# Optimization experiments

Hardware: AMD Instinct MI355X
Metric: run time of the kernel (lower is better)

## Reference

```python
import jax, jax.numpy as jnp
import numpy as np

NUM_GRAPHS = 512


def setup_inputs() -> dict:
    key = jax.random.key(0)
    ks = jax.random.split(key, 16)
    N, E = 50000, 800000
    x = jax.random.normal(ks[0], (N, 3), dtype=jnp.float32)
    edge_index = jax.random.randint(ks[1], (2, E), 0, N, dtype=jnp.int64)
    batch = jnp.sort(jax.random.randint(ks[2], (N,), 0, NUM_GRAPHS, dtype=jnp.int64))

    def glorot(k, shape):
        fan_in, fan_out = shape
        lim = (6.0 / (fan_in + fan_out)) ** 0.5
        return jax.random.uniform(k, shape, jnp.float32, -lim, lim)

    return {
        "x": x, "edge_index": edge_index, "batch": batch,
        "W1": glorot(ks[3], (3, 32)),   "b1": jnp.zeros((32,), jnp.float32),
        "W2": glorot(ks[4], (32, 64)),  "b2": jnp.zeros((64,), jnp.float32),
        "W3": glorot(ks[5], (64, 128)), "b3": jnp.zeros((128,), jnp.float32),
        "Wf1": glorot(ks[6], (128, 32)), "bf1": jnp.zeros((32,), jnp.float32),
        "Wf2": glorot(ks[7], (32, 4)),   "bf2": jnp.zeros((4,), jnp.float32),
    }


def _gcn_conv(x, src, dst, norm, W, b, N):
    # GCNConv: h = x W, then symmetric-normalized aggregation, then bias.
    h = x @ W                                   # [N, out]
    msg = h[src] * norm[:, None]                # [E+N, out] gathered edge messages
    out = jax.ops.segment_sum(msg, dst, num_segments=N)
    return out + b


def reference(x, edge_index, batch, W1, b1, W2, b2, W3, b3, Wf1, bf1, Wf2, bf2):
    N = x.shape[0]
    loops = jnp.arange(N, dtype=edge_index.dtype)
    src = jnp.concatenate([edge_index[0], loops])   # add self-loops (GCNConv default)
    dst = jnp.concatenate([edge_index[1], loops])
    # symmetric normalization deg^-1/2[src] * deg^-1/2[dst], deg counted on dst
    deg = jax.ops.segment_sum(jnp.ones_like(dst, dtype=x.dtype), dst, num_segments=N)
    dinv = jnp.where(deg > 0, jax.lax.rsqrt(deg), 0.0)
    norm = dinv[src] * dinv[dst]                    # [E+N]

    h = jax.nn.relu(_gcn_conv(x, src, dst, norm, W1, b1, N))
    h = jax.nn.relu(_gcn_conv(h, src, dst, norm, W2, b2, N))
    h = jax.nn.relu(_gcn_conv(h, src, dst, norm, W3, b3, N))

    # global mean pool over graphs
    sums = jax.ops.segment_sum(h, batch, num_segments=NUM_GRAPHS)
    cnts = jax.ops.segment_sum(jnp.ones((N,), h.dtype), batch, num_segments=NUM_GRAPHS)
    pooled = sums / jnp.maximum(cnts, 1.0)[:, None]   # [G, 128]

    z = jax.nn.relu(pooled @ Wf1 + bf1)
    return z @ Wf2 + bf2                              # [G, 4]
```

## Files before the change

kernel.cpp:

```cpp
#include <hip/hip_runtime.h>

#define NN 50000
#define NE 800000
#define NG 512
#define CAP 64
#define NP 196
#define CH 3200
#define NCH 250

__global__ __launch_bounds__(256) void p1_hist_k(const int* __restrict__ dst,
                                                 int* __restrict__ Ht, int e) {
    __shared__ int lh[NP];
    int t = threadIdx.x, b = blockIdx.x;
    if (t < NP) lh[t] = 0;
    __syncthreads();
    int i0 = b * CH, i1 = min(e, i0 + CH);
    for (int i = i0 + t; i < i1; i += 256) atomicAdd(&lh[dst[i] >> 8], 1);
    __syncthreads();
    if (t < NP) Ht[t * NCH + b] = lh[t];
}

__global__ __launch_bounds__(256) void p2a_k(int* __restrict__ Ht, int* __restrict__ tot) {
    __shared__ int sh[256];
    int p = blockIdx.x, t = threadIdx.x;
    int v = (t < NCH) ? Ht[p * NCH + t] : 0;
    sh[t] = v;
    __syncthreads();
    for (int off = 1; off < 256; off <<= 1) {
        int x = (t >= off) ? sh[t - off] : 0;
        __syncthreads();
        sh[t] += x;
        __syncthreads();
    }
    if (t < NCH) Ht[p * NCH + t] = sh[t] - v;
    if (t == 255) tot[p] = sh[255];
}

__global__ __launch_bounds__(256) void p2b_k(const int* __restrict__ tot,
                                             int* __restrict__ start) {
    __shared__ int sh[256];
    int t = threadIdx.x;
    int v = (t < NP) ? tot[t] : 0;
    sh[t] = v;
    __syncthreads();
    for (int off = 1; off < 256; off <<= 1) {
        int x = (t >= off) ? sh[t - off] : 0;
        __syncthreads();
        sh[t] += x;
        __syncthreads();
    }
    if (t < NP) start[t] = sh[t] - v;
    if (t == 255) start[NP] = sh[255];
}

__global__ __launch_bounds__(256) void p3_place_k(const int* __restrict__ src,
                                                  const int* __restrict__ dst,
                                                  const int* __restrict__ Ht,
                                                  const int* __restrict__ start,
                                                  int* __restrict__ pak, int e) {
    __shared__ int cur[NP];
    int t = threadIdx.x, b = blockIdx.x;
    if (t < NP) cur[t] = start[t] + Ht[t * NCH + b];
    __syncthreads();
    int i0 = b * CH, i1 = min(e, i0 + CH);
    for (int i = i0 + t; i < i1; i += 256) {
        int d = dst[i], s = src[i];
        int p = d >> 8, dl = d & 255;
        int pos = atomicAdd(&cur[p], 1);
        pak[pos] = s | (dl << 16);
    }
}

__global__ __launch_bounds__(256) void p4_build_k(const int* __restrict__ pak,
                                                  const int* __restrict__ start,
                                                  const float* __restrict__ x,
                                                  int* __restrict__ fill,
                                                  float* __restrict__ dinv,
                                                  float* __restrict__ xs,
                                                  int* __restrict__ eidx, int n) {
    __shared__ int lh[256], curn[256];
    int p = blockIdx.x, t = threadIdx.x;
    lh[t] = 0;
    curn[t] = 0;
    __syncthreads();
    int s0 = start[p], s1 = start[p + 1];
    for (int i = s0 + t; i < s1; i += 256) atomicAdd(&lh[pak[i] >> 16], 1);
    __syncthreads();
    int node = p * 256 + t;
    if (node < n) {
        int dg = lh[t];
        fill[node] = dg;
        float d = rsqrtf((float)(dg + 1));
        dinv[node] = d;
        float4 v;
        v.x = x[node * 3 + 0] * d;
        v.y = x[node * 3 + 1] * d;
        v.z = x[node * 3 + 2] * d;
        v.w = 0.0f;
        *(float4*)(xs + (size_t)node * 4) = v;
    }
    __syncthreads();
    for (int i = s0 + t; i < s1; i += 256) {
        int w = pak[i];
        int dl = w >> 16, s = w & 0xFFFF;
        int pos = atomicAdd(&curn[dl], 1) & (CAP - 1);
        eidx[(size_t)(p * 256 + dl) * CAP + pos] = s;
    }
}

__device__ __forceinline__ unsigned short f2bf_rn(float f) {
    unsigned int u = __float_as_uint(f);
    u += 0x7FFFu + ((u >> 16) & 1u);
    return (unsigned short)(u >> 16);
}

__global__ __launch_bounds__(256) void fused_l1_k(
    const int* __restrict__ deg, const int* __restrict__ eidx,
    const float* __restrict__ xs, const float* __restrict__ W1,
    const float* __restrict__ b1, const float* __restrict__ dinv,
    float* __restrict__ A2, unsigned short* __restrict__ A2b, int n) {
    __shared__ float act[64][4];
    int t = threadIdx.x;
    int node0 = blockIdx.x * 64;
    {
        int node = node0 + (t >> 2);
        int f = t & 3;
        if (node < n) {
            int e1 = deg[node];
            const int* __restrict__ eb = eidx + node * CAP;
            float acc = xs[(size_t)node * 4 + f];
            int e = 0;
            for (; e + 4 <= e1; e += 4) {
                int4 s = *(const int4*)(eb + e);
                float v0 = xs[(size_t)s.x * 4 + f];
                float v1 = xs[(size_t)s.y * 4 + f];
                float v2 = xs[(size_t)s.z * 4 + f];
                float v3 = xs[(size_t)s.w * 4 + f];
                acc += (v0 + v1) + (v2 + v3);
            }
            for (; e < e1; ++e) acc += xs[(size_t)eb[e] * 4 + f];
            act[t >> 2][f] = acc;
        }
    }
    __syncthreads();
    int f = t & 31;
    int nl0 = t >> 5;
#pragma unroll
    for (int i = 0; i < 8; ++i) {
        int nl = nl0 + i * 8;
        int node = node0 + nl;
        if (node < n) {
            float acc = act[nl][0] * W1[f] + act[nl][1] * W1[32 + f] + act[nl][2] * W1[64 + f];
            float s = dinv[node];
            float o = fmaxf(fmaf(s, acc, b1[f]), 0.0f) * s;
            A2[(size_t)node * 32 + f] = o;
            A2b[(size_t)node * 32 + f] = f2bf_rn(o);
        }
    }
}

template <int F>
__global__ __launch_bounds__(256) void gatherbf_k(const int* __restrict__ deg,
                                                  const int* __restrict__ eidx,
                                                  const float* __restrict__ Aself,
                                                  const uint4* __restrict__ Ab,
                                                  float* __restrict__ B, int n) {
    constexpr int FV = F / 8;
    constexpr int NPB = 256 / FV;
    constexpr int RU4 = F / 8;
    int t = threadIdx.x;
    int node = blockIdx.x * NPB + t / FV;
    int j = (t % FV) * 8;
    if (node >= n) return;
    int e1 = deg[node];
    const int* __restrict__ eb = eidx + (size_t)node * CAP;
    const uint4* __restrict__ Aj = Ab + (j >> 3);
    float4 p0 = *(const float4*)(Aself + (size_t)node * F + j);
    float4 p1 = *(const float4*)(Aself + (size_t)node * F + j + 4);
    float4 q0 = make_float4(0.f, 0.f, 0.f, 0.f);
    float4 q1 = make_float4(0.f, 0.f, 0.f, 0.f);
#define BF_UNPACK8(u, lo, hi)                                                 \
    {                                                                         \
        lo.x += __uint_as_float((u).x << 16);                                 \
        lo.y += __uint_as_float((u).x & 0xFFFF0000u);                         \
        lo.z += __uint_as_float((u).y << 16);                                 \
        lo.w += __uint_as_float((u).y & 0xFFFF0000u);                         \
        hi.x += __uint_as_float((u).z << 16);                                 \
        hi.y += __uint_as_float((u).z & 0xFFFF0000u);                         \
        hi.z += __uint_as_float((u).w << 16);                                 \
        hi.w += __uint_as_float((u).w & 0xFFFF0000u);                         \
    }
    int e = 0;
    for (; e + 16 <= e1; e += 16) {
        int4 sa = *(const int4*)(eb + e);
        int4 sb = *(const int4*)(eb + e + 4);
        int4 sc = *(const int4*)(eb + e + 8);
        int4 sd = *(const int4*)(eb + e + 12);
        uint4 v0 = Aj[(size_t)sa.x * RU4];
        uint4 v1 = Aj[(size_t)sa.y * RU4];
        uint4 v2 = Aj[(size_t)sa.z * RU4];
        uint4 v3 = Aj[(size_t)sa.w * RU4];
        uint4 v4 = Aj[(size_t)sb.x * RU4];
        uint4 v5 = Aj[(size_t)sb.y * RU4];
        uint4 v6 = Aj[(size_t)sb.z * RU4];
        uint4 v7 = Aj[(size_t)sb.w * RU4];
        uint4 v8 = Aj[(size_t)sc.x * RU4];
        uint4 v9 = Aj[(size_t)sc.y * RU4];
        uint4 va = Aj[(size_t)sc.z * RU4];
        uint4 vb = Aj[(size_t)sc.w * RU4];
        uint4 vc = Aj[(size_t)sd.x * RU4];
        uint4 vd = Aj[(size_t)sd.y * RU4];
        uint4 ve = Aj[(size_t)sd.z * RU4];
        uint4 vf = Aj[(size_t)sd.w * RU4];
        BF_UNPACK8(v0, p0, p1) BF_UNPACK8(v1, q0, q1)
        BF_UNPACK8(v2, p0, p1) BF_UNPACK8(v3, q0, q1)
        BF_UNPACK8(v4, p0, p1) BF_UNPACK8(v5, q0, q1)
        BF_UNPACK8(v6, p0, p1) BF_UNPACK8(v7, q0, q1)
        BF_UNPACK8(v8, p0, p1) BF_UNPACK8(v9, q0, q1)
        BF_UNPACK8(va, p0, p1) BF_UNPACK8(vb, q0, q1)
        BF_UNPACK8(vc, p0, p1) BF_UNPACK8(vd, q0, q1)
        BF_UNPACK8(ve, p0, p1) BF_UNPACK8(vf, q0, q1)
    }
    for (; e + 4 <= e1; e += 4) {
        int4 sa = *(const int4*)(eb + e);
        uint4 v0 = Aj[(size_t)sa.x * RU4];
        uint4 v1 = Aj[(size_t)sa.y * RU4];
        uint4 v2 = Aj[(size_t)sa.z * RU4];
        uint4 v3 = Aj[(size_t)sa.w * RU4];
        BF_UNPACK8(v0, p0, p1) BF_UNPACK8(v1, q0, q1)
        BF_UNPACK8(v2, p0, p1) BF_UNPACK8(v3, q0, q1)
    }
    for (; e < e1; ++e) {
        uint4 v = Aj[(size_t)eb[e] * RU4];
        BF_UNPACK8(v, p0, p1)
    }
#undef BF_UNPACK8
    p0.x += q0.x; p0.y += q0.y; p0.z += q0.z; p0.w += q0.w;
    p1.x += q1.x; p1.y += q1.y; p1.z += q1.z; p1.w += q1.w;
    *(float4*)(B + (size_t)node * F + j) = p0;
    *(float4*)(B + (size_t)node * F + j + 4) = p1;
}

template <int Fin, int Fout, int NPB, bool SCALE_OUT, bool WRITE_BF>
__global__ __launch_bounds__(256) void mmB_k(
    const float* __restrict__ G, const float* __restrict__ W,
    const float* __restrict__ bias, const float* __restrict__ dinv,
    float* __restrict__ Aout, unsigned short* __restrict__ Abf, int n) {
    constexpr int FL = Fout / 4;
    constexpr int NGRP = 256 / FL;
    constexpr int NPT = NPB / NGRP;
    __shared__ float act[NPB][Fin];
    int t = threadIdx.x;
    int node0 = blockIdx.x * NPB;
    constexpr int TOT4 = NPB * Fin / 4;
    const float4* __restrict__ G4 = (const float4*)(G + (size_t)node0 * Fin);
    float4* act4 = (float4*)&act[0][0];
    for (int i = t; i < TOT4; i += 256) {
        int nl = i / (Fin / 4);
        float4 v = make_float4(0.f, 0.f, 0.f, 0.f);
        if (node0 + nl < n) v = G4[i];
        act4[i] = v;
    }
    __syncthreads();
    int f4 = (t % FL) * 4;
    int nlbase = (t / FL) * NPT;
    float4 acc[NPT];
#pragma unroll
    for (int i = 0; i < NPT; ++i) acc[i] = make_float4(0.f, 0.f, 0.f, 0.f);
    for (int k = 0; k < Fin; k += 4) {
        float4 a[NPT];
#pragma unroll
        for (int i = 0; i < NPT; ++i) a[i] = *(const float4*)&act[nlbase + i][k];
#pragma unroll
        for (int kk = 0; kk < 4; ++kk) {
            float4 w = *(const float4*)(W + (size_t)(k + kk) * Fout + f4);
#pragma unroll
            for (int i = 0; i < NPT; ++i) {
                float av = (&a[i].x)[kk];
                acc[i].x = fmaf(av, w.x, acc[i].x);
                acc[i].y = fmaf(av, w.y, acc[i].y);
                acc[i].z = fmaf(av, w.z, acc[i].z);
                acc[i].w = fmaf(av, w.w, acc[i].w);
            }
        }
    }
    float4 bv = *(const float4*)(bias + f4);
#pragma unroll
    for (int i = 0; i < NPT; ++i) {
        int node = node0 + nlbase + i;
        if (node < n) {
            float s = dinv[node];
            float4 o;
            o.x = fmaxf(fmaf(s, acc[i].x, bv.x), 0.0f);
            o.y = fmaxf(fmaf(s, acc[i].y, bv.y), 0.0f);
            o.z = fmaxf(fmaf(s, acc[i].z, bv.z), 0.0f);
            o.w = fmaxf(fmaf(s, acc[i].w, bv.w), 0.0f);
            if (SCALE_OUT) { o.x *= s; o.y *= s; o.z *= s; o.w *= s; }
            *(float4*)(Aout + (size_t)node * Fout + f4) = o;
            if (WRITE_BF) {
                ushort4 ob;
                ob.x = f2bf_rn(o.x); ob.y = f2bf_rn(o.y);
                ob.z = f2bf_rn(o.z); ob.w = f2bf_rn(o.w);
                *(ushort4*)(Abf + (size_t)node * Fout + f4) = ob;
            }
        }
    }
}

__device__ __forceinline__ int lbound_d(const int* __restrict__ a, int n, int key) {
    int lo = 0, hi = n;
    while (lo < hi) {
        int m = (lo + hi) >> 1;
        if (a[m] < key) lo = m + 1; else hi = m;
    }
    return lo;
}

__global__ __launch_bounds__(128) void poolhead_k(
    const float* __restrict__ H, const int* __restrict__ batch,
    const float* __restrict__ Wf1, const float* __restrict__ bf1,
    const float* __restrict__ Wf2, const float* __restrict__ bf2,
    float* __restrict__ out, int n) {
    __shared__ int bnd[2];
    __shared__ float pm[128];
    __shared__ float z[32];
    int g = blockIdx.x, t = threadIdx.x;
    if (t == 0) bnd[0] = lbound_d(batch, n, g);
    if (t == 1) bnd[1] = lbound_d(batch, n, g + 1);
    __syncthreads();
    int lo = bnd[0], hi = bnd[1];
    float s0 = 0.f, s1 = 0.f, s2 = 0.f, s3 = 0.f;
    int i = lo;
    for (; i + 4 <= hi; i += 4) {
        s0 += H[(size_t)i * 128 + t];
        s1 += H[(size_t)(i + 1) * 128 + t];
        s2 += H[(size_t)(i + 2) * 128 + t];
        s3 += H[(size_t)(i + 3) * 128 + t];
    }
    for (; i < hi; ++i) s0 += H[(size_t)i * 128 + t];
    float c = (float)(hi - lo);
    c = fmaxf(c, 1.0f);
    pm[t] = ((s0 + s1) + (s2 + s3)) / c;
    __syncthreads();
    if (t < 32) {
        float acc = bf1[t];
#pragma unroll 4
        for (int k = 0; k < 128; ++k) acc = fmaf(pm[k], Wf1[k * 32 + t], acc);
        z[t] = fmaxf(acc, 0.0f);
    }
    __syncthreads();
    if (t < 4) {
        float acc = bf2[t];
#pragma unroll
        for (int jj = 0; jj < 32; ++jj) acc = fmaf(z[jj], Wf2[jj * 4 + t], acc);
        out[g * 4 + t] = acc;
    }
}

extern "C" void kernel_launch(void* const* d_in, const int* in_sizes, int n_in,
                              void* d_out, int out_size, void* d_ws, size_t ws_size,
                              hipStream_t stream) {
    const float* x    = (const float*)d_in[0];
    const int*   ei   = (const int*)d_in[1];
    const int*   batch= (const int*)d_in[2];
    const float* W1   = (const float*)d_in[3];
    const float* b1   = (const float*)d_in[4];
    const float* W2   = (const float*)d_in[5];
    const float* b2   = (const float*)d_in[6];
    const float* W3   = (const float*)d_in[7];
    const float* b3   = (const float*)d_in[8];
    const float* Wf1  = (const float*)d_in[9];
    const float* bf1  = (const float*)d_in[10];
    const float* Wf2  = (const float*)d_in[11];
    const float* bf2  = (const float*)d_in[12];
    float* out = (float*)d_out;

    int*   fill   = (int*)d_ws;
    float* dinv   = (float*)(fill + NN);
    float* xs     = dinv + NN;
    float* A2     = xs + (size_t)NN * 4;
    float* A3     = A2 + (size_t)NN * 32;
    float* H3     = A3 + (size_t)NN * 64;
    float* G      = H3 + (size_t)NN * 128;
    int*   eidx   = (int*)(G + (size_t)NN * 64);
    unsigned short* A3b = (unsigned short*)(eidx + (size_t)NN * CAP);
    unsigned short* A2b = A3b + (size_t)NN * 64;

    int* pak   = (int*)G;
    int* Ht    = (int*)H3;
    int* tot   = Ht + NP * NCH;
    int* start = tot + 256;

    const int* src = ei;
    const int* dst = ei + NE;

    p1_hist_k<<<NCH, 256, 0, stream>>>(dst, Ht, NE);
    p2a_k<<<NP, 256, 0, stream>>>(Ht, tot);
    p2b_k<<<1, 256, 0, stream>>>(tot, start);
    p3_place_k<<<NCH, 256, 0, stream>>>(src, dst, Ht, start, pak, NE);
    p4_build_k<<<NP, 256, 0, stream>>>(pak, start, x, fill, dinv, xs, eidx, NN);

    fused_l1_k<<<(NN + 63) / 64, 256, 0, stream>>>(
        fill, eidx, xs, W1, b1, dinv, A2, A2b, NN);

    gatherbf_k<32><<<(NN + 63) / 64, 256, 0, stream>>>(
        fill, eidx, A2, (const uint4*)A2b, G, NN);
    mmB_k<32, 64, 32, true, true><<<(NN + 31) / 32, 256, 0, stream>>>(
        G, W2, b2, dinv, A3, A3b, NN);

    gatherbf_k<64><<<(NN + 31) / 32, 256, 0, stream>>>(
        fill, eidx, A3, (const uint4*)A3b, G, NN);
    mmB_k<64, 128, 32, false, false><<<(NN + 31) / 32, 256, 0, stream>>>(
        G, W3, b3, dinv, H3, (unsigned short*)nullptr, NN);

    poolhead_k<<<NG, 128, 0, stream>>>(H3, batch, Wf1, bf1, Wf2, bf2, out, NN);
}
```

Baseline: 209.1 us.

## Split 64-wide bf16 features into halves and gather from bf16 self term

The layer-3 gather now runs as two passes over 32-feature halves, each stored as its own bf16 array, so each gathered table is half the size and fits better in cache. The self-loop term is read from the bf16 copy instead of a separate fp32 array, so the fp32 A2/A3 activations are no longer written at all. In exchange there is an extra kernel launch, the edge lists are read twice, and the self term loses precision.

```diff
diff --git a/kernel.cpp b/kernel.cpp
--- a/kernel.cpp
+++ b/kernel.cpp
@@ -118,7 +118,7 @@
     const int* __restrict__ deg, const int* __restrict__ eidx,
     const float* __restrict__ xs, const float* __restrict__ W1,
     const float* __restrict__ b1, const float* __restrict__ dinv,
-    float* __restrict__ A2, unsigned short* __restrict__ A2b, int n) {
+    unsigned short* __restrict__ A2b, int n) {
     __shared__ float act[64][4];
     int t = threadIdx.x;
     int node0 = blockIdx.x * 64;
@@ -153,30 +153,25 @@
             float acc = act[nl][0] * W1[f] + act[nl][1] * W1[32 + f] + act[nl][2] * W1[64 + f];
             float s = dinv[node];
             float o = fmaxf(fmaf(s, acc, b1[f]), 0.0f) * s;
-            A2[(size_t)node * 32 + f] = o;
             A2b[(size_t)node * 32 + f] = f2bf_rn(o);
         }
     }
 }
 
-template <int F>
-__global__ __launch_bounds__(256) void gatherbf_k(const int* __restrict__ deg,
-                                                  const int* __restrict__ eidx,
-                                                  const float* __restrict__ Aself,
-                                                  const uint4* __restrict__ Ab,
-                                                  float* __restrict__ B, int n) {
-    constexpr int FV = F / 8;
-    constexpr int NPB = 256 / FV;
-    constexpr int RU4 = F / 8;
+template <int GSTRIDE, int GOFF>
+__global__ __launch_bounds__(256) void gatherbfH_k(const int* __restrict__ deg,
+                                                   const int* __restrict__ eidx,
+                                                   const uint4* __restrict__ Ab,
+                                                   float* __restrict__ B, int n) {
     int t = threadIdx.x;
-    int node = blockIdx.x * NPB + t / FV;
-    int j = (t % FV) * 8;
+    int node = blockIdx.x * 64 + (t >> 2);
+    int j = (t & 3) * 8;
     if (node >= n) return;
     int e1 = deg[node];
     const int* __restrict__ eb = eidx + (size_t)node * CAP;
     const uint4* __restrict__ Aj = Ab + (j >> 3);
-    float4 p0 = *(const float4*)(Aself + (size_t)node * F + j);
-    float4 p1 = *(const float4*)(Aself + (size_t)node * F + j + 4);
+    float4 p0 = make_float4(0.f, 0.f, 0.f, 0.f);
+    float4 p1 = make_float4(0.f, 0.f, 0.f, 0.f);
     float4 q0 = make_float4(0.f, 0.f, 0.f, 0.f);
     float4 q1 = make_float4(0.f, 0.f, 0.f, 0.f);
 #define BF_UNPACK8(u, lo, hi)                                                 \
@@ -190,28 +185,32 @@
         hi.z += __uint_as_float((u).w << 16);                                 \
         hi.w += __uint_as_float((u).w & 0xFFFF0000u);                         \
     }
+    {
+        uint4 sv = Aj[(size_t)node * 4];
+        BF_UNPACK8(sv, p0, p1)
+    }
     int e = 0;
     for (; e + 16 <= e1; e += 16) {
         int4 sa = *(const int4*)(eb + e);
         int4 sb = *(const int4*)(eb + e + 4);
         int4 sc = *(const int4*)(eb + e + 8);
         int4 sd = *(const int4*)(eb + e + 12);
-        uint4 v0 = Aj[(size_t)sa.x * RU4];
-        uint4 v1 = Aj[(size_t)sa.y * RU4];
-        uint4 v2 = Aj[(size_t)sa.z * RU4];
-        uint4 v3 = Aj[(size_t)sa.w * RU4];
-        uint4 v4 = Aj[(size_t)sb.x * RU4];
-        uint4 v5 = Aj[(size_t)sb.y * RU4];
-        uint4 v6 = Aj[(size_t)sb.z * RU4];
-        uint4 v7 = Aj[(size_t)sb.w * RU4];
-        uint4 v8 = Aj[(size_t)sc.x * RU4];
-        uint4 v9 = Aj[(size_t)sc.y * RU4];
-        uint4 va = Aj[(size_t)sc.z * RU4];
-        uint4 vb = Aj[(size_t)sc.w * RU4];
-        uint4 vc = Aj[(size_t)sd.x * RU4];
-        uint4 vd = Aj[(size_t)sd.y * RU4];
-        uint4 ve = Aj[(size_t)sd.z * RU4];
-        uint4 vf = Aj[(size_t)sd.w * RU4];
+        uint4 v0 = Aj[(size_t)sa.x * 4];
+        uint4 v1 = Aj[(size_t)sa.y * 4];
+        uint4 v2 = Aj[(size_t)sa.z * 4];
+        uint4 v3 = Aj[(size_t)sa.w * 4];
+        uint4 v4 = Aj[(size_t)sb.x * 4];
+        uint4 v5 = Aj[(size_t)sb.y * 4];
+        uint4 v6 = Aj[(size_t)sb.z * 4];
+        uint4 v7 = Aj[(size_t)sb.w * 4];
+        uint4 v8 = Aj[(size_t)sc.x * 4];
+        uint4 v9 = Aj[(size_t)sc.y * 4];
+        uint4 va = Aj[(size_t)sc.z * 4];
+        uint4 vb = Aj[(size_t)sc.w * 4];
+        uint4 vc = Aj[(size_t)sd.x * 4];
+        uint4 vd = Aj[(size_t)sd.y * 4];
+        uint4 ve = Aj[(size_t)sd.z * 4];
+        uint4 vf = Aj[(size_t)sd.w * 4];
         BF_UNPACK8(v0, p0, p1) BF_UNPACK8(v1, q0, q1)
         BF_UNPACK8(v2, p0, p1) BF_UNPACK8(v3, q0, q1)
         BF_UNPACK8(v4, p0, p1) BF_UNPACK8(v5, q0, q1)
@@ -223,29 +222,31 @@
     }
     for (; e + 4 <= e1; e += 4) {
         int4 sa = *(const int4*)(eb + e);
-        uint4 v0 = Aj[(size_t)sa.x * RU4];
-        uint4 v1 = Aj[(size_t)sa.y * RU4];
-        uint4 v2 = Aj[(size_t)sa.z * RU4];
-        uint4 v3 = Aj[(size_t)sa.w * RU4];
+        uint4 v0 = Aj[(size_t)sa.x * 4];
+        uint4 v1 = Aj[(size_t)sa.y * 4];
+        uint4 v2 = Aj[(size_t)sa.z * 4];
+        uint4 v3 = Aj[(size_t)sa.w * 4];
         BF_UNPACK8(v0, p0, p1) BF_UNPACK8(v1, q0, q1)
         BF_UNPACK8(v2, p0, p1) BF_UNPACK8(v3, q0, q1)
     }
     for (; e < e1; ++e) {
-        uint4 v = Aj[(size_t)eb[e] * RU4];
+        uint4 v = Aj[(size_t)eb[e] * 4];
         BF_UNPACK8(v, p0, p1)
     }
 #undef BF_UNPACK8
     p0.x += q0.x; p0.y += q0.y; p0.z += q0.z; p0.w += q0.w;
     p1.x += q1.x; p1.y += q1.y; p1.z += q1.z; p1.w += q1.w;
-    *(float4*)(B + (size_t)node * F + j) = p0;
-    *(float4*)(B + (size_t)node * F + j + 4) = p1;
-}
-
-template <int Fin, int Fout, int NPB, bool SCALE_OUT, bool WRITE_BF>
+    float* __restrict__ Bo = B + (size_t)node * GSTRIDE + GOFF + j;
+    *(float4*)(Bo) = p0;
+    *(float4*)(Bo + 4) = p1;
+}
+
+template <int Fin, int Fout, int NPB, bool SCALE_OUT, bool SPLIT_BF>
 __global__ __launch_bounds__(256) void mmB_k(
     const float* __restrict__ G, const float* __restrict__ W,
     const float* __restrict__ bias, const float* __restrict__ dinv,
-    float* __restrict__ Aout, unsigned short* __restrict__ Abf, int n) {
+    float* __restrict__ Aout, unsigned short* __restrict__ AbfL,
+    unsigned short* __restrict__ AbfH, int n) {
     constexpr int FL = Fout / 4;
     constexpr int NGRP = 256 / FL;
     constexpr int NPT = NPB / NGRP;
@@ -296,12 +297,14 @@
             o.z = fmaxf(fmaf(s, acc[i].z, bv.z), 0.0f);
             o.w = fmaxf(fmaf(s, acc[i].w, bv.w), 0.0f);
             if (SCALE_OUT) { o.x *= s; o.y *= s; o.z *= s; o.w *= s; }
-            *(float4*)(Aout + (size_t)node * Fout + f4) = o;
-            if (WRITE_BF) {
+            if (SPLIT_BF) {
                 ushort4 ob;
                 ob.x = f2bf_rn(o.x); ob.y = f2bf_rn(o.y);
                 ob.z = f2bf_rn(o.z); ob.w = f2bf_rn(o.w);
-                *(ushort4*)(Abf + (size_t)node * Fout + f4) = ob;
+                if (f4 < 32) *(ushort4*)(AbfL + (size_t)node * 32 + f4) = ob;
+                else         *(ushort4*)(AbfH + (size_t)node * 32 + (f4 - 32)) = ob;
+            } else {
+                *(float4*)(Aout + (size_t)node * Fout + f4) = o;
             }
         }
     }
@@ -378,13 +381,12 @@
     int*   fill   = (int*)d_ws;
     float* dinv   = (float*)(fill + NN);
     float* xs     = dinv + NN;
-    float* A2     = xs + (size_t)NN * 4;
-    float* A3     = A2 + (size_t)NN * 32;
-    float* H3     = A3 + (size_t)NN * 64;
-    float* G      = H3 + (size_t)NN * 128;
-    int*   eidx   = (int*)(G + (size_t)NN * 64);
-    unsigned short* A3b = (unsigned short*)(eidx + (size_t)NN * CAP);
-    unsigned short* A2b = A3b + (size_t)NN * 64;
+    float* G      = xs + (size_t)NN * 4;
+    float* H3     = G + (size_t)NN * 64;
+    int*   eidx   = (int*)(H3 + (size_t)NN * 128);
+    unsigned short* A2b  = (unsigned short*)(eidx + (size_t)NN * CAP);
+    unsigned short* A3bL = A2b + (size_t)NN * 32;
+    unsigned short* A3bH = A3bL + (size_t)NN * 32;
 
     int* pak   = (int*)G;
     int* Ht    = (int*)H3;
@@ -401,17 +403,19 @@
     p4_build_k<<<NP, 256, 0, stream>>>(pak, start, x, fill, dinv, xs, eidx, NN);
 
     fused_l1_k<<<(NN + 63) / 64, 256, 0, stream>>>(
-        fill, eidx, xs, W1, b1, dinv, A2, A2b, NN);
-
-    gatherbf_k<32><<<(NN + 63) / 64, 256, 0, stream>>>(
-        fill, eidx, A2, (const uint4*)A2b, G, NN);
+        fill, eidx, xs, W1, b1, dinv, A2b, NN);
+
+    gatherbfH_k<32, 0><<<(NN + 63) / 64, 256, 0, stream>>>(
+        fill, eidx, (const uint4*)A2b, G, NN);
     mmB_k<32, 64, 32, true, true><<<(NN + 31) / 32, 256, 0, stream>>>(
-        G, W2, b2, dinv, A3, A3b, NN);
-
-    gatherbf_k<64><<<(NN + 31) / 32, 256, 0, stream>>>(
-        fill, eidx, A3, (const uint4*)A3b, G, NN);
+        G, W2, b2, dinv, nullptr, A3bL, A3bH, NN);
+
+    gatherbfH_k<64, 0><<<(NN + 63) / 64, 256, 0, stream>>>(
+        fill, eidx, (const uint4*)A3bL, G, NN);
+    gatherbfH_k<64, 32><<<(NN + 63) / 64, 256, 0, stream>>>(
+        fill, eidx, (const uint4*)A3bH, G, NN);
     mmB_k<64, 128, 32, false, false><<<(NN + 31) / 32, 256, 0, stream>>>(
-        G, W3, b3, dinv, H3, (unsigned short*)nullptr, NN);
+        G, W3, b3, dinv, H3, nullptr, nullptr, NN);
 
     poolhead_k<<<NG, 128, 0, stream>>>(H3, batch, Wf1, bf1, Wf2, bf2, out, NN);
 }
```

Measured after the change: 212.8 us. About the same (+1.7%).

## Fold prefix scan into placement kernels, drop degree pass, store final layer as bf16

Applied to the files above, without the earlier changes.

Removes the single-block p2b scan kernel by recomputing the 196-entry prefix scan redundantly inside p3_place_k and p4_build_k. p4_build_k no longer does a separate histogram pass over the packed edges; it takes degrees from the per-node insertion counters after the scatter. The last GCN layer now writes only a bf16 copy of its 128-wide output, and the pooling kernel reads that instead of fp32. This cuts one launch, one pass over the packed edges and half the final-layer traffic, at the cost of redundant scan work per block and bf16 rounding in the pooled sums.

```diff
diff --git a/kernel.cpp b/kernel.cpp
--- a/kernel.cpp
+++ b/kernel.cpp
@@ -36,31 +36,24 @@
     if (t == 255) tot[p] = sh[255];
 }
 
-__global__ __launch_bounds__(256) void p2b_k(const int* __restrict__ tot,
-                                             int* __restrict__ start) {
-    __shared__ int sh[256];
-    int t = threadIdx.x;
-    int v = (t < NP) ? tot[t] : 0;
-    sh[t] = v;
-    __syncthreads();
-    for (int off = 1; off < 256; off <<= 1) {
-        int x = (t >= off) ? sh[t - off] : 0;
-        __syncthreads();
-        sh[t] += x;
-        __syncthreads();
-    }
-    if (t < NP) start[t] = sh[t] - v;
-    if (t == 255) start[NP] = sh[255];
-}
-
 __global__ __launch_bounds__(256) void p3_place_k(const int* __restrict__ src,
                                                   const int* __restrict__ dst,
                                                   const int* __restrict__ Ht,
-                                                  const int* __restrict__ start,
+                                                  const int* __restrict__ tot,
                                                   int* __restrict__ pak, int e) {
     __shared__ int cur[NP];
+    __shared__ int sh[256];
     int t = threadIdx.x, b = blockIdx.x;
-    if (t < NP) cur[t] = start[t] + Ht[t * NCH + b];
+    int v = (t < NP) ? tot[t] : 0;
+    sh[t] = v;
+    __syncthreads();
+    for (int off = 1; off < 256; off <<= 1) {
+        int x = (t >= off) ? sh[t - off] : 0;
+        __syncthreads();
+        sh[t] += x;
+        __syncthreads();
+    }
+    if (t < NP) cur[t] = (sh[t] - v) + Ht[t * NCH + b];
     __syncthreads();
     int i0 = b * CH, i1 = min(e, i0 + CH);
     for (int i = i0 + t; i < i1; i += 256) {
@@ -72,39 +65,45 @@
 }
 
 __global__ __launch_bounds__(256) void p4_build_k(const int* __restrict__ pak,
-                                                  const int* __restrict__ start,
+                                                  const int* __restrict__ tot,
                                                   const float* __restrict__ x,
                                                   int* __restrict__ fill,
                                                   float* __restrict__ dinv,
                                                   float* __restrict__ xs,
                                                   int* __restrict__ eidx, int n) {
-    __shared__ int lh[256], curn[256];
+    __shared__ int curn[256], sh[256];
     int p = blockIdx.x, t = threadIdx.x;
-    lh[t] = 0;
     curn[t] = 0;
-    __syncthreads();
-    int s0 = start[p], s1 = start[p + 1];
-    for (int i = s0 + t; i < s1; i += 256) atomicAdd(&lh[pak[i] >> 16], 1);
-    __syncthreads();
-    int node = p * 256 + t;
-    if (node < n) {
-        int dg = lh[t];
-        fill[node] = dg;
-        float d = rsqrtf((float)(dg + 1));
-        dinv[node] = d;
-        float4 v;
-        v.x = x[node * 3 + 0] * d;
-        v.y = x[node * 3 + 1] * d;
-        v.z = x[node * 3 + 2] * d;
-        v.w = 0.0f;
-        *(float4*)(xs + (size_t)node * 4) = v;
-    }
-    __syncthreads();
+    int v = (t < NP) ? tot[t] : 0;
+    sh[t] = v;
+    __syncthreads();
+    for (int off = 1; off < 256; off <<= 1) {
+        int x2 = (t >= off) ? sh[t - off] : 0;
+        __syncthreads();
+        sh[t] += x2;
+        __syncthreads();
+    }
+    int s1 = sh[p];
+    int s0 = s1 - tot[p];
     for (int i = s0 + t; i < s1; i += 256) {
         int w = pak[i];
         int dl = w >> 16, s = w & 0xFFFF;
         int pos = atomicAdd(&curn[dl], 1) & (CAP - 1);
         eidx[(size_t)(p * 256 + dl) * CAP + pos] = s;
+    }
+    __syncthreads();
+    int node = p * 256 + t;
+    if (node < n) {
+        int dg = curn[t];
+        fill[node] = dg;
+        float d = rsqrtf((float)(dg + 1));
+        dinv[node] = d;
+        float4 vv;
+        vv.x = x[node * 3 + 0] * d;
+        vv.y = x[node * 3 + 1] * d;
+        vv.z = x[node * 3 + 2] * d;
+        vv.w = 0.0f;
+        *(float4*)(xs + (size_t)node * 4) = vv;
     }
 }
 
@@ -241,7 +240,7 @@
     *(float4*)(B + (size_t)node * F + j + 4) = p1;
 }
 
-template <int Fin, int Fout, int NPB, bool SCALE_OUT, bool WRITE_BF>
+template <int Fin, int Fout, int NPB, bool SCALE_OUT, bool WRITE_F32, bool WRITE_BF>
 __global__ __launch_bounds__(256) void mmB_k(
     const float* __restrict__ G, const float* __restrict__ W,
     const float* __restrict__ bias, const float* __restrict__ dinv,
@@ -296,7 +295,7 @@
             o.z = fmaxf(fmaf(s, acc[i].z, bv.z), 0.0f);
             o.w = fmaxf(fmaf(s, acc[i].w, bv.w), 0.0f);
             if (SCALE_OUT) { o.x *= s; o.y *= s; o.z *= s; o.w *= s; }
-            *(float4*)(Aout + (size_t)node * Fout + f4) = o;
+            if (WRITE_F32) *(float4*)(Aout + (size_t)node * Fout + f4) = o;
             if (WRITE_BF) {
                 ushort4 ob;
                 ob.x = f2bf_rn(o.x); ob.y = f2bf_rn(o.y);
@@ -317,7 +316,7 @@
 }
 
 __global__ __launch_bounds__(128) void poolhead_k(
-    const float* __restrict__ H, const int* __restrict__ batch,
+    const unsigned short* __restrict__ Hb, const int* __restrict__ batch,
     const float* __restrict__ Wf1, const float* __restrict__ bf1,
     const float* __restrict__ Wf2, const float* __restrict__ bf2,
     float* __restrict__ out, int n) {
@@ -332,12 +331,12 @@
     float s0 = 0.f, s1 = 0.f, s2 = 0.f, s3 = 0.f;
     int i = lo;
     for (; i + 4 <= hi; i += 4) {
-        s0 += H[(size_t)i * 128 + t];
-        s1 += H[(size_t)(i + 1) * 128 + t];
-        s2 += H[(size_t)(i + 2) * 128 + t];
-        s3 += H[(size_t)(i + 3) * 128 + t];
-    }
-    for (; i < hi; ++i) s0 += H[(size_t)i * 128 + t];
+        s0 += __uint_as_float((unsigned)Hb[(size_t)i * 128 + t] << 16);
+        s1 += __uint_as_float((unsigned)Hb[(size_t)(i + 1) * 128 + t] << 16);
+        s2 += __uint_as_float((unsigned)Hb[(size_t)(i + 2) * 128 + t] << 16);
+        s3 += __uint_as_float((unsigned)Hb[(size_t)(i + 3) * 128 + t] << 16);
+    }
+    for (; i < hi; ++i) s0 += __uint_as_float((unsigned)Hb[(size_t)i * 128 + t] << 16);
     float c = (float)(hi - lo);
     c = fmaxf(c, 1.0f);
     pm[t] = ((s0 + s1) + (s2 + s3)) / c;
@@ -380,38 +379,36 @@
     float* xs     = dinv + NN;
     float* A2     = xs + (size_t)NN * 4;
     float* A3     = A2 + (size_t)NN * 32;
-    float* H3     = A3 + (size_t)NN * 64;
-    float* G      = H3 + (size_t)NN * 128;
+    float* G      = A3 + (size_t)NN * 64;
     int*   eidx   = (int*)(G + (size_t)NN * 64);
-    unsigned short* A3b = (unsigned short*)(eidx + (size_t)NN * CAP);
-    unsigned short* A2b = A3b + (size_t)NN * 64;
-
-    int* pak   = (int*)G;
-    int* Ht    = (int*)H3;
-    int* tot   = Ht + NP * NCH;
-    int* start = tot + 256;
+    unsigned short* A2b = (unsigned short*)(eidx + (size_t)NN * CAP);
+    unsigned short* A3b = A2b + (size_t)NN * 32;
+    unsigned short* H3b = A3b + (size_t)NN * 64;
+
+    int* pak = (int*)G;
+    int* Ht  = (int*)H3b;
+    int* tot = Ht + NP * NCH;
 
     const int* src = ei;
     const int* dst = ei + NE;
 
     p1_hist_k<<<NCH, 256, 0, stream>>>(dst, Ht, NE);
     p2a_k<<<NP, 256, 0, stream>>>(Ht, tot);
-    p2b_k<<<1, 256, 0, stream>>>(tot, start);
-    p3_place_k<<<NCH, 256, 0, stream>>>(src, dst, Ht, start, pak, NE);
-    p4_build_k<<<NP, 256, 0, stream>>>(pak, start, x, fill, dinv, xs, eidx, NN);
+    p3_place_k<<<NCH, 256, 0, stream>>>(src, dst, Ht, tot, pak, NE);
+    p4_build_k<<<NP, 256, 0, stream>>>(pak, tot, x, fill, dinv, xs, eidx, NN);
 
     fused_l1_k<<<(NN + 63) / 64, 256, 0, stream>>>(
         fill, eidx, xs, W1, b1, dinv, A2, A2b, NN);
 
     gatherbf_k<32><<<(NN + 63) / 64, 256, 0, stream>>>(
         fill, eidx, A2, (const uint4*)A2b, G, NN);
-    mmB_k<32, 64, 32, true, true><<<(NN + 31) / 32, 256, 0, stream>>>(
+    mmB_k<32, 64, 32, true, true, true><<<(NN + 31) / 32, 256, 0, stream>>>(
         G, W2, b2, dinv, A3, A3b, NN);
 
     gatherbf_k<64><<<(NN + 31) / 32, 256, 0, stream>>>(
         fill, eidx, A3, (const uint4*)A3b, G, NN);
-    mmB_k<64, 128, 32, false, false><<<(NN + 31) / 32, 256, 0, stream>>>(
-        G, W3, b3, dinv, H3, (unsigned short*)nullptr, NN);
-
-    poolhead_k<<<NG, 128, 0, stream>>>(H3, batch, Wf1, bf1, Wf2, bf2, out, NN);
-}
+    mmB_k<64, 128, 32, false, false, true><<<(NN + 31) / 32, 256, 0, stream>>>(
+        G, W3, b3, dinv, nullptr, H3b, NN);
+
+    poolhead_k<<<NG, 128, 0, stream>>>(H3b, batch, Wf1, bf1, Wf2, bf2, out, NN);
+}
```

After: 205.2 us. Within noise of the previous version (-1.9%).
